# Kernel optimization log

Hardware: AMD Instinct MI355X
Metric: run time of the kernel (lower is better)

Reference implementation:

```python
import jax, jax.numpy as jnp
import numpy as np

# Dimensions
NT, NS = 1000, 2048   # timesteps, basins
NF, NG = 6, 32        # forcing channels, static attributes
NH, NR, HS = 16, 8, 256  # buckets, routing taps, hidden size
NK, NGD = 3, 9        # len(kDict)=3 (km,ki,ke), len(gDict)=9


def setup_inputs() -> dict:
    key = jax.random.key(0)
    ks = jax.random.split(key, 16)
    # Physically plausible forcings: Prcp/Evp nonnegative, T1<=T2 (min/max temp)
    Prcp = jax.random.uniform(ks[0], (NT, NS)) * 10.0
    Evp = jax.random.uniform(ks[1], (NT, NS)) * 5.0
    Tm = jax.random.normal(ks[2], (NT, NS)) * 10.0
    T1 = Tm - jax.random.uniform(ks[3], (NT, NS)) * 5.0
    T2 = Tm + jax.random.uniform(ks[4], (NT, NS)) * 5.0
    Rad = jax.random.uniform(ks[5], (NT, NS))
    Hum = jax.random.uniform(ks[6], (NT, NS))
    x = jnp.stack([Prcp, Evp, T1, T2, Rad, Hum], axis=-1)  # [nt, ns, 6]
    xc = jax.random.normal(ks[7], (NS, NG))

    def lin(k, fan_in, fan_out, s=0.05):
        k1, k2 = jax.random.split(k)
        return (jax.random.normal(k1, (fan_in, fan_out)) * s,
                jax.random.normal(k2, (fan_out,)) * s)

    W_fc, b_fc = lin(ks[8], NG, HS)
    W_r, b_r = lin(ks[9], HS, NH * (NR + 1))
    W_g, b_g = lin(ks[10], HS, NH * NGD)
    W_kin, b_kin = lin(ks[11], 4, HS)
    W_kout, b_kout = lin(ks[12], HS, NH * NK)
    return dict(x=x, xc=xc, W_fc=W_fc, b_fc=b_fc, W_r=W_r, b_r=b_r,
                W_g=W_g, b_g=b_g, W_kin=W_kin, b_kin=b_kin,
                W_kout=W_kout, b_kout=b_kout)


def _hardsigmoid(v):
    return jnp.clip(v / 6.0 + 0.5, 0.0, 1.0)


def _forward(x, xc, W_fc, b_fc, W_r, b_r, W_g, b_g, W_kin, b_kin, W_kout, b_kout):
    nt, ns, _ = x.shape
    Prcp, Evp, T1, T2 = x[..., 0], x[..., 1], x[..., 2], x[..., 3]
    f = x[..., 2:]                        # [nt, ns, 4] (T1,T2,Rad,Hum)

    # ---- getParam (eval mode: DropMask is identity) ----
    state = xc @ W_fc + b_fc              # [ns, hs]
    pK = jnp.tanh(f @ W_kin + b_kin + state) @ W_kout + b_kout  # [nt, ns, nh*3]
    hG = jnp.tanh(state)
    pG = hG @ W_g + b_g                   # [ns, nh*9]
    pR = hG @ W_r + b_r                   # [ns, nh*(nr+1)]

    # sepParam(K): km=exp, ki=relu, ke=exp  -> time-varying [nt, ns, nh]
    km = jnp.exp(pK[..., 0 * NH:1 * NH])
    ki = jax.nn.relu(pK[..., 1 * NH:2 * NH])
    ke = jnp.exp(pK[..., 2 * NH:3 * NH])

    # sepParam(G): static [ns, nh]
    g = lambda i: pG[..., i * NH:(i + 1) * NH]
    kp = jax.nn.sigmoid(g(0))
    ks_ = jax.nn.sigmoid(g(1))
    kd = jax.nn.sigmoid(g(2))
    gd = jax.nn.sigmoid(g(3))
    gl = (jax.nn.sigmoid(g(4)) * 10.0) ** 3
    qb = jax.nn.relu(g(5)) / 10.0
    ga = jax.nn.softmax(g(6), axis=-1)    # area weights over buckets
    gi = _hardsigmoid(g(7)) / 2.0
    ge = jax.nn.relu(g(8))

    # onePeakWeight: unimodal routing weights [ns, nh, nr]
    r = pR.reshape(ns, NH, NR + 1)
    s = jax.nn.softmax(r, axis=-1)
    c = jnp.cumsum(s, axis=-1)
    w = jnp.minimum(c, 1.0 - c + s)[..., :NR]
    wr = w / jnp.sum(w, axis=-1, keepdims=True)

    # divideP: snow/liquid split from min/max temperature crossing 0 C
    fl = jnp.clip(T2 / (T2 - T1 + 1e-5), 0.0, 1.0)  # liquid fraction
    Pl = (Prcp * fl)[..., None]           # [nt, ns, 1]
    Ps = (Prcp * (1.0 - fl))[..., None]
    Ev = Evp[..., None]

    # ---- bucket.step recurrence over time (the custom-scan hot loop) ----
    def step(carry, inp):
        Sf, Ss, Sg = carry                # each [ns, nh]
        Ps_t, Pl_t, Ev_t, km_t, ki_t, ke_t = inp
        # snow bucket: accumulate, melt capped by degree-day factor km
        Sf = Sf + Ps_t
        qf = jnp.minimum(Sf, km_t)
        Sf = Sf - qf
        # partition inflow: impervious/direct fraction gi
        inflow = qf + Pl_t
        qd = inflow * gi
        Ss = Ss + inflow * (1.0 - gi)
        # evapotranspiration
        E = jnp.minimum(jnp.maximum(Ss, 0.0), Ev_t * ke_t * ge)
        Ss = Ss - E
        # interflow capped by ki
        qi = jnp.minimum(ki_t, jnp.maximum(Ss, 0.0))
        Ss = Ss - qi
        # quick flow above capacity gl, slow drainage below
        qp = kp * jnp.maximum(Ss - gl, 0.0)
        qsa = ks_ * jnp.clip(Ss, 0.0, gl)
        Ss = Ss - qp - qsa
        # deep/groundwater bucket: fraction gd percolates, linear reservoir kd + baseflow qb
        Sg = Sg + qsa * gd
        qg = kd * Sg + qb
        Sg = Sg * (1.0 - kd)
        q = qp + qsa * (1.0 - gd) + qg + qd + qi
        return (Sf, Ss, Sg), q

    init = (jnp.zeros((ns, NH), x.dtype),
            jnp.zeros((ns, NH), x.dtype),
            jnp.zeros((ns, NH), x.dtype))
    _, Qp = jax.lax.scan(step, init, (Ps, Pl, Ev, km, ki, ke))  # [nt, ns, nh]

    # routing: valid temporal convolution with per-bucket unit hydrograph wr
    Tout = nt - NR + 1
    Q = jnp.zeros((Tout, ns, NH), Qp.dtype)
    for rr in range(NR):  # NR is a small fixed constant
        Q = Q + Qp[NR - 1 - rr: nt - rr] * wr[..., rr]
    yOut = jnp.sum(Q * ga, axis=-1)       # [Tout, ns]
    return yOut


def reference(x, xc, W_fc, b_fc, W_r, b_r, W_g, b_g, W_kin, b_kin, W_kout, b_kout):
    return _forward(x, xc, W_fc, b_fc, W_r, b_r, W_g, b_g, W_kin, b_kin, W_kout, b_kout)
```

## Files before the change

kernel.cpp:

```cpp
#include <hip/hip_runtime.h>
#include <hip/hip_bf16.h>

#define NT   1000
#define NS   2048
#define NH   16
#define NR   8
#define HS   256
#define TOUT 993

typedef __attribute__((ext_vector_type(8))) short short8;
typedef __attribute__((ext_vector_type(4))) float f32x4;

__device__ __forceinline__ ushort f2bf(float f) {
    union { float f; unsigned int u; } v; v.f = f;
    unsigned int u = v.u;
    return (ushort)((u + 0x7fffu + ((u >> 16) & 1u)) >> 16);
}
__device__ __forceinline__ float bf2f(ushort u) {
    union { unsigned int i; float f; } v; v.i = ((unsigned int)u) << 16; return v.f;
}
__device__ __forceinline__ unsigned int packbf2(float lo, float hi) {
    union { __hip_bfloat162 b; unsigned int u; } v;
    v.b = __float22bfloat162_rn(make_float2(lo, hi));
    return v.u;
}
__device__ __forceinline__ float sigf(float x) { return 1.f / (1.f + __expf(-x)); }
__device__ __forceinline__ float fast_tanh(float z) {
    float e = exp2f(z * 2.885390082f);
    return 1.f - 2.f * __builtin_amdgcn_rcpf(e + 1.f);
}
template<int CTRL>
__device__ __forceinline__ float dpp_add(float v) {
    int s = __builtin_amdgcn_update_dpp(0, __builtin_bit_cast(int, v), CTRL, 0xf, 0xf, true);
    return v + __builtin_bit_cast(float, s);
}
__device__ __forceinline__ void gll16(const void* g, void* l) {
    __builtin_amdgcn_global_load_lds((const __attribute__((address_space(1))) unsigned int*)g,
                                     (__attribute__((address_space(3))) unsigned int*)l, 16, 0, 0);
}
__device__ __forceinline__ void gll4(const void* g, void* l) {
    __builtin_amdgcn_global_load_lds((const __attribute__((address_space(1))) unsigned int*)g,
                                     (__attribute__((address_space(3))) unsigned int*)l, 4, 0, 0);
}

__global__ __launch_bounds__(256) void kA(
    const float* __restrict__ xc, const float* __restrict__ W_fc, const float* __restrict__ b_fc,
    const float* __restrict__ W_r, const float* __restrict__ b_r,
    const float* __restrict__ W_g, const float* __restrict__ b_g,
    const float* __restrict__ W_kin, const float* __restrict__ b_kin,
    const float* __restrict__ W_kout,
    float* __restrict__ stateK, float* __restrict__ params,
    ushort* __restrict__ Wt_g, ushort* __restrict__ whlo_g)
{
    __shared__ float xcs[32];
    __shared__ float hG[256];
    __shared__ float pGR[288];
    const int s = blockIdx.x, tid = threadIdx.x;

    if (tid < 32) xcs[tid] = xc[s * 32 + tid];
    __syncthreads();

    float acc = b_fc[tid];
#pragma unroll 8
    for (int k = 0; k < 32; ++k) acc = fmaf(xcs[k], W_fc[k * 256 + tid], acc);
    stateK[s * 256 + tid] = acc + b_kin[tid];
    hG[tid] = tanhf(acc);
    __syncthreads();

    for (int j = tid; j < 288; j += 256) {
        const float* W = (j < 144) ? W_g : W_r;
        const float* b = (j < 144) ? b_g : b_r;
        int col = (j < 144) ? j : (j - 144);
        float a = b[col];
#pragma unroll 4
        for (int k = 0; k < 256; ++k) a = fmaf(hG[k], W[k * 144 + col], a);
        pGR[j] = a;
    }
    __syncthreads();

    if (tid < 16) {
        const int h = tid;
        float g0 = pGR[h],       g1 = pGR[16 + h],  g2 = pGR[32 + h];
        float g3 = pGR[48 + h],  g4 = pGR[64 + h],  g5 = pGR[80 + h];
        float g6 = pGR[96 + h],  g7 = pGR[112 + h], g8 = pGR[128 + h];
        float kp = sigf(g0), ksg = sigf(g1), kd = sigf(g2), gd = sigf(g3);
        float t4 = sigf(g4) * 10.f; float gl = t4 * t4 * t4;
        float qb = fmaxf(g5, 0.f) * 0.1f;
        float gi = fminf(fmaxf(g7 * (1.f / 6.f) + 0.5f, 0.f), 1.f) * 0.5f;
        float ge = fmaxf(g8, 0.f);
        float m = g6;
        for (int o = 1; o < 16; o <<= 1) m = fmaxf(m, __shfl_xor(m, o));
        float e = __expf(g6 - m), esum = e;
        for (int o = 1; o < 16; o <<= 1) esum += __shfl_xor(esum, o);
        float ga = e / esum;
        float r[9], rm = -1e30f;
#pragma unroll
        for (int i = 0; i < 9; ++i) { r[i] = pGR[144 + h * 9 + i]; rm = fmaxf(rm, r[i]); }
        float er[9], es = 0.f;
#pragma unroll
        for (int i = 0; i < 9; ++i) { er[i] = __expf(r[i] - rm); es += er[i]; }
        float inv_es = 1.f / es, c = 0.f, wsum = 0.f, w[8];
#pragma unroll
        for (int i = 0; i < 8; ++i) {
            float si = er[i] * inv_es; c += si;
            float wi = fminf(c, 1.f - c + si);
            w[i] = wi; wsum += wi;
        }
        const int base = s * 16 + h;
        params[0 * 32768 + base] = kp;       params[1 * 32768 + base] = ksg;
        params[2 * 32768 + base] = kd;       params[3 * 32768 + base] = gd;
        params[4 * 32768 + base] = gl;       params[5 * 32768 + base] = qb;
        params[6 * 32768 + base] = gi;       params[7 * 32768 + base] = 1.f - gi;
        params[8 * 32768 + base] = 1.f - kd; params[9 * 32768 + base] = 1.f - gd;
        params[10 * 32768 + base] = ge;
        float sc = ga / wsum;
#pragma unroll
        for (int i = 0; i < 8; ++i) params[(11 + i) * 32768 + base] = w[i] * sc;
    }

    if (s == 0) {
        for (int i = tid; i < 48 * 256; i += 256) {
            int col = i % 48, slot = i / 48;
            int kk = slot >> 5, q = (slot >> 3) & 3, j = slot & 7;
            int h = kk * 32 + ((j < 4) ? (q * 4 + j) : (16 + q * 4 + (j - 4)));
            Wt_g[col * 264 + slot] = f2bf(W_kout[h * 48 + col]);
        }
        {
            const int h = tid;
#pragma unroll
            for (int f = 0; f < 4; ++f) {
                float w = W_kin[f * 256 + h];
                ushort hi = f2bf(w);
                float lo = w - bf2f(hi);
                whlo_g[h * 8 + f] = hi;
                whlo_g[h * 8 + 4 + f] = f2bf(lo);
            }
        }
    }
}

__global__ __launch_bounds__(256, 3) void kB(
    const float* __restrict__ x,
    const float* __restrict__ stateK, const float* __restrict__ b_kout,
    const ushort* __restrict__ Wt_g, const ushort* __restrict__ whlo_g,
    const float* __restrict__ params,
    unsigned int* __restrict__ kmki, ushort* __restrict__ kevA,
    float2* __restrict__ pspl)
{
    __shared__ ushort Wt[48 * 264];
    __shared__ float  stS[16 * 260];
    __shared__ ushort whloS[2048];
    __shared__ float  geS[256];
    __shared__ float  evS[4][5][16];
    const int tid = threadIdx.x;
    const int st = blockIdx.x & 127;
    const int tg = blockIdx.x >> 7;
    const int s0 = st << 4;

    for (int i = tid; i < 3168; i += 256)
        ((uint2*)Wt)[i] = ((const uint2*)Wt_g)[i];
#pragma unroll
    for (int i = tid; i < 1024; i += 256) {
        int row = i >> 6, c = (i & 63) << 2;
        *(float4*)(stS + row * 260 + c) = *(const float4*)(stateK + (s0 + row) * 256 + c);
    }
    *(float4*)(whloS + tid * 8) = ((const float4*)whlo_g)[tid];
    geS[tid] = params[10 * 32768 + s0 * 16 + tid];
    __syncthreads();

    const int wv = tid >> 6, lane = tid & 63;
    const int mi = lane & 15, quad = lane >> 4;
    const int site = s0 + mi;
    const int t0 = tg * 20 + wv * 5;

    float xf[5][4];
#pragma unroll
    for (int ti = 0; ti < 5; ++ti) {
        const int t = t0 + ti;
        const int xb = (t * 2048 + site) * 6;
        float2 u23 = *(const float2*)(x + xb + 2);
        float2 u45 = *(const float2*)(x + xb + 4);
        xf[ti][0] = u23.x; xf[ti][1] = u23.y; xf[ti][2] = u45.x; xf[ti][3] = u45.y;
        if (lane < 16) {
            float2 u01 = *(const float2*)(x + xb);
            float fl = fminf(fmaxf(u23.y * __builtin_amdgcn_rcpf(u23.y - u23.x + 1e-5f), 0.f), 1.f);
            const int sg = st * 4 + (mi >> 2), sl = mi & 3;
            pspl[(sg * 1000 + t) * 4 + sl] = make_float2(u01.x * (1.f - fl), u01.x * fl);
            evS[wv][ti][mi] = u01.y;
        }
    }

    unsigned int bfr[5][4];
#pragma unroll
    for (int ti = 0; ti < 5; ++ti) {
        const float x0 = xf[ti][0], x1 = xf[ti][1], x2 = xf[ti][2], x3 = xf[ti][3];
        unsigned int h01 = packbf2(x0, x1), h23 = packbf2(x2, x3);
        float l0 = x0 - bf2f((ushort)(h01 & 0xffffu));
        float l1 = x1 - bf2f((ushort)(h01 >> 16));
        float l2 = x2 - bf2f((ushort)(h23 & 0xffffu));
        float l3 = x3 - bf2f((ushort)(h23 >> 16));
        unsigned int l01 = packbf2(l0, l1), l23 = packbf2(l2, l3);
        bfr[ti][0] = (quad == 0) ? h01 : (quad == 1 ? l01 : 0u);
        bfr[ti][1] = (quad == 0) ? h23 : (quad == 1 ? l23 : 0u);
        bfr[ti][2] = (quad == 0) ? h01 : 0u;
        bfr[ti][3] = (quad == 0) ? h23 : 0u;
    }

    const float*  stp = stS + mi * 260;
    const ushort* Wt0 = Wt + mi * 264 + quad * 8;
    const int q4 = quad * 4;

    f32x4 acc[5][3];
#pragma unroll
    for (int ti = 0; ti < 5; ++ti)
#pragma unroll
        for (int j = 0; j < 3; ++j) acc[ti][j] = (f32x4){0.f, 0.f, 0.f, 0.f};

#pragma unroll 1
    for (int kk = 0; kk < 8; ++kk) {
        const int ko = kk * 32;
        union { short8 s; unsigned int u[4]; } W0, W1, A0, A1;
        W0.s = *(const short8*)(whloS + (ko + mi) * 8);
        W1.s = *(const short8*)(whloS + (ko + 16 + mi) * 8);
        A0.u[0] = (quad <= 1) ? W0.u[0] : 0u;
        A0.u[1] = (quad <= 1) ? W0.u[1] : 0u;
        A0.u[2] = (quad == 0) ? W0.u[2] : 0u;
        A0.u[3] = (quad == 0) ? W0.u[3] : 0u;
        A1.u[0] = (quad <= 1) ? W1.u[0] : 0u;
        A1.u[1] = (quad <= 1) ? W1.u[1] : 0u;
        A1.u[2] = (quad == 0) ? W1.u[2] : 0u;
        A1.u[3] = (quad == 0) ? W1.u[3] : 0u;
        f32x4 c0 = *(const f32x4*)(stp + ko + q4);
        f32x4 c1 = *(const f32x4*)(stp + ko + 16 + q4);
        short8 b0 = *(const short8*)(Wt0 + ko);
        short8 b1 = *(const short8*)(Wt0 + 16 * 264 + ko);
        short8 b2 = *(const short8*)(Wt0 + 32 * 264 + ko);
#pragma unroll
        for (int ti = 0; ti < 5; ++ti) {
            union { short8 s; unsigned int u[4]; } B;
            B.u[0] = bfr[ti][0]; B.u[1] = bfr[ti][1];
            B.u[2] = bfr[ti][2]; B.u[3] = bfr[ti][3];
            f32x4 z0 = __builtin_amdgcn_mfma_f32_16x16x32_bf16(A0.s, B.s, c0, 0, 0, 0);
            f32x4 z1 = __builtin_amdgcn_mfma_f32_16x16x32_bf16(A1.s, B.s, c1, 0, 0, 0);
            union { short8 s; unsigned int u[4]; } a;
            a.u[0] = packbf2(fast_tanh(z0[0]), fast_tanh(z0[1]));
            a.u[1] = packbf2(fast_tanh(z0[2]), fast_tanh(z0[3]));
            a.u[2] = packbf2(fast_tanh(z1[0]), fast_tanh(z1[1]));
            a.u[3] = packbf2(fast_tanh(z1[2]), fast_tanh(z1[3]));
            acc[ti][0] = __builtin_amdgcn_mfma_f32_16x16x32_bf16(a.s, b0, acc[ti][0], 0, 0, 0);
            acc[ti][1] = __builtin_amdgcn_mfma_f32_16x16x32_bf16(a.s, b1, acc[ti][1], 0, 0, 0);
            acc[ti][2] = __builtin_amdgcn_mfma_f32_16x16x32_bf16(a.s, b2, acc[ti][2], 0, 0, 0);
        }
    }

    const float bo0 = b_kout[mi], bo1 = b_kout[16 + mi], bo2 = b_kout[32 + mi];
#pragma unroll
    for (int ti = 0; ti < 5; ++ti) {
        const int t = t0 + ti;
#pragma unroll
        for (int reg = 0; reg < 4; ++reg) {
            const int sl = quad * 4 + reg;
            float km = __expf(acc[ti][0][reg] + bo0);
            float ki = fmaxf(acc[ti][1][reg] + bo1, 0.f);
            float ke = __expf(acc[ti][2][reg] + bo2);
            float kev = ke * evS[wv][ti][sl] * geS[sl * 16 + mi];
            const int idx = ((s0 + sl) * 1000 + t) * 16 + mi;
            kmki[idx] = (unsigned int)f2bf(km) | ((unsigned int)f2bf(ki) << 16);
            kevA[idx] = f2bf(kev);
        }
    }
}

#define KM_STRIDE 4160
#define KE_BASE   16640
#define KE_STRIDE 2080
#define PS_BASE   24960
#define BUF_SZ    27008
__global__ __launch_bounds__(64, 1) void kC(
    const unsigned int* __restrict__ kmki, const ushort* __restrict__ kevA,
    const float2* __restrict__ pspl,
    const float* __restrict__ params, float* __restrict__ yOut)
{
    __shared__ char lds[2 * BUF_SZ];
    const int tid = threadIdx.x;
    const int sg = blockIdx.x;
    const int sl = tid >> 4;
    const int s = sg * 4 + sl;
    const int h = tid & 15;
    const int gid = s * 16 + h;

    const float kp  = params[0 * 32768 + gid];
    const float ks_ = params[1 * 32768 + gid];
    const float kd  = params[2 * 32768 + gid];
    const float gd  = params[3 * 32768 + gid];
    const float gl  = params[4 * 32768 + gid];
    const float qbv = params[5 * 32768 + gid];
    const float gi  = params[6 * 32768 + gid];
    const float gi1 = params[7 * 32768 + gid];
    const float kd1 = params[8 * 32768 + gid];
    const float gd1 = params[9 * 32768 + gid];
    float wrga[8];
#pragma unroll
    for (int i = 0; i < 8; ++i) wrga[i] = params[(11 + i) * 32768 + gid];

    float Sf = 0.f, Ss = 0.f, Sg = 0.f;
    float qcur[8], qp1[8], qp2[8];
#pragma unroll
    for (int i = 0; i < 8; ++i) { qcur[i] = 0.f; qp1[i] = 0.f; qp2[i] = 0.f; }

    const char* kmG = (const char*)kmki;
    const char* keG = (const char*)kevA;
    const char* psG = (const char*)pspl;

#define STAGE(c, TAIL) do {                                                     \
        char* L = lds + ((c) & 1) * BUF_SZ;                                     \
        _Pragma("unroll")                                                       \
        for (int q = 0; q < 4; ++q) {                                           \
            const char* gk = kmG + ((size_t)(sg * 4 + q) * 1000 + (c) * 64) * 64; \
            const char* ge = keG + ((size_t)(sg * 4 + q) * 1000 + (c) * 64) * 32; \
            char* lk = L + q * KM_STRIDE;                                       \
            char* le = L + KE_BASE + q * KE_STRIDE;                             \
            if (!(TAIL)) {                                                      \
                _Pragma("unroll")                                               \
                for (int k = 0; k < 4; ++k) gll16(gk + k * 1024 + tid * 16, lk + k * 1024); \
                _Pragma("unroll")                                               \
                for (int k = 0; k < 2; ++k) gll16(ge + k * 1024 + tid * 16, le + k * 1024); \
            } else {                                                            \
                _Pragma("unroll")                                               \
                for (int k = 0; k < 2; ++k) gll16(gk + k * 1024 + tid * 16, lk + k * 1024); \
                _Pragma("unroll")                                               \
                for (int k = 0; k < 2; ++k) gll4(gk + 2048 + k * 256 + tid * 4, lk + 2048 + k * 256); \
                gll16(ge + tid * 16, le);                                       \
                gll4(ge + 1024 + tid * 4, le + 1024);                           \
            }                                                                   \
        }                                                                       \
        const char* gp = psG + ((size_t)sg * 1000 + (c) * 64) * 32;             \
        char* lp = L + PS_BASE;                                                 \
        if (!(TAIL)) { gll16(gp + tid * 16, lp); gll16(gp + 1024 + tid * 16, lp + 1024); } \
        else         { gll16(gp + tid * 16, lp); gll4(gp + 1024 + tid * 4, lp + 1024); }   \
    } while (0)

#define SCANB(c, sb) do {                                                       \
        const char* L = lds + ((c) & 1) * BUF_SZ;                               \
        const char* lk = L + sl * KM_STRIDE + h * 4 + (sb) * 512;               \
        const char* le = L + KE_BASE + sl * KE_STRIDE + h * 2 + (sb) * 256;     \
        const char* lp = L + PS_BASE + sl * 8 + (sb) * 256;                     \
        unsigned int a[8]; ushort e[8]; float2 p[8];                            \
        _Pragma("unroll")                                                       \
        for (int i = 0; i < 8; ++i) {                                           \
            a[i] = *(const unsigned int*)(lk + i * 64);                         \
            e[i] = *(const ushort*)(le + i * 32);                               \
            p[i] = *(const float2*)(lp + i * 32);                               \
        }                                                                       \
        _Pragma("unroll")                                                       \
        for (int i = 0; i < 8; ++i) {                                           \
            float km = __builtin_bit_cast(float, a[i] << 16);                   \
            float ki = __builtin_bit_cast(float, a[i] & 0xffff0000u);           \
            float kev = __builtin_bit_cast(float, ((unsigned int)e[i]) << 16);  \
            float ps = p[i].x, pl = p[i].y;                                     \
            Sf += ps;                                                           \
            float qf = fminf(Sf, km); Sf -= qf;                                 \
            float inflow = qf + pl;                                             \
            float qd = inflow * gi;                                             \
            Ss = fmaf(inflow, gi1, Ss);                                         \
            float E = fminf(Ss, kev); Ss -= E;                                  \
            float qi = fminf(ki, Ss); Ss -= qi;                                 \
            float qp = kp * fmaxf(Ss - gl, 0.f);                                \
            float qsa = ks_ * fminf(Ss, gl);                                    \
            Ss -= qp + qsa;                                                     \
            Sg = fmaf(qsa, gd, Sg);                                             \
            float qg = fmaf(kd, Sg, qbv);                                       \
            Sg *= kd1;                                                          \
            qcur[i] = fmaf(qsa, gd1, qp) + qg + qd + qi;                        \
        }                                                                       \
    } while (0)

#define CONV_STORE(m) do {                                                      \
        float z[8];                                                             \
        _Pragma("unroll")                                                       \
        for (int i = 0; i < 8; ++i) {                                           \
            float za = wrga[6] * ((i >= 6) ? qp1[i - 6] : qp2[i + 2]);          \
            za = fmaf(wrga[4], (i >= 4) ? qp1[i - 4] : qp2[i + 4], za);         \
            za = fmaf(wrga[2], (i >= 2) ? qp1[i - 2] : qp2[i + 6], za);         \
            za = fmaf(wrga[0], qp1[i], za);                                     \
            float zb = wrga[7] * ((i >= 7) ? qp1[i - 7] : qp2[i + 1]);          \
            zb = fmaf(wrga[5], (i >= 5) ? qp1[i - 5] : qp2[i + 3], zb);         \
            zb = fmaf(wrga[3], (i >= 3) ? qp1[i - 3] : qp2[i + 5], zb);         \
            zb = fmaf(wrga[1], (i >= 1) ? qp1[i - 1] : qp2[i + 7], zb);         \
            z[i] = za + zb;                                                     \
        }                                                                       \
        _Pragma("unroll")                                                       \
        for (int i = 0; i < 8; ++i) z[i] = dpp_add<0xB1>(z[i]);                 \
        _Pragma("unroll")                                                       \
        for (int i = 0; i < 8; ++i) z[i] = dpp_add<0x4E>(z[i]);                 \
        _Pragma("unroll")                                                       \
        for (int i = 0; i < 8; ++i) z[i] = dpp_add<0x141>(z[i]);                \
        _Pragma("unroll")                                                       \
        for (int i = 0; i < 8; ++i) z[i] = dpp_add<0x140>(z[i]);                \
        if (h == 0) {                                                           \
            _Pragma("unroll")                                                   \
            for (int i = 0; i < 8; ++i) {                                       \
                const int t = (m) * 8 + i;                                      \
                if (t >= 7) yOut[(t - 7) * 2048 + s] = z[i];                    \
            }                                                                   \
        }                                                                       \
    } while (0)

    STAGE(0, false);
    int g = 0;
#pragma unroll 1
    for (int c = 0; c < 16; ++c) {
        if (c < 15) {
            if (c + 1 == 15) STAGE(15, true);
            else             STAGE(c + 1, false);
            asm volatile("s_waitcnt vmcnt(26)" ::: "memory");
        } else {
            asm volatile("s_waitcnt vmcnt(0)" ::: "memory");
        }
        const int NSB = (c == 15) ? 5 : 8;
#pragma unroll 1
        for (int sb = 0; sb < NSB; ++sb, ++g) {
            SCANB(c, sb);
            CONV_STORE(g - 1);
#pragma unroll
            for (int i = 0; i < 8; ++i) { qp2[i] = qp1[i]; qp1[i] = qcur[i]; }
        }
        asm volatile("" ::: "memory");
    }
    CONV_STORE(124);
#undef STAGE
#undef SCANB
#undef CONV_STORE
}

extern "C" void kernel_launch(void* const* d_in, const int* in_sizes, int n_in,
                              void* d_out, int out_size, void* d_ws, size_t ws_size,
                              hipStream_t stream) {
    const float* x      = (const float*)d_in[0];
    const float* xc     = (const float*)d_in[1];
    const float* W_fc   = (const float*)d_in[2];
    const float* b_fc   = (const float*)d_in[3];
    const float* W_r    = (const float*)d_in[4];
    const float* b_r    = (const float*)d_in[5];
    const float* W_g    = (const float*)d_in[6];
    const float* b_g    = (const float*)d_in[7];
    const float* W_kin  = (const float*)d_in[8];
    const float* b_kin  = (const float*)d_in[9];
    const float* W_kout = (const float*)d_in[10];
    const float* b_kout = (const float*)d_in[11];
    float* yOut = (float*)d_out;

    char* ws = (char*)d_ws;
    float*  stateK = (float*)(ws + 0);
    float*  params = (float*)(ws + (2 << 20));
    ushort* Wt_g   = (ushort*)(ws + (6 << 20));
    ushort* whlo_g = (ushort*)(ws + (6 << 20) + (64 << 10));
    char*   p      = ws + (6 << 20) + (128 << 10);
    float2* pspl   = (float2*)p;
    unsigned int* kmki = (unsigned int*)(p + 16384000);
    ushort* kevA   = (ushort*)(p + 16384000 + 131072000);

    hipLaunchKernelGGL(kA, dim3(2048), dim3(256), 0, stream,
                       xc, W_fc, b_fc, W_r, b_r, W_g, b_g, W_kin, b_kin, W_kout,
                       stateK, params, Wt_g, whlo_g);
    hipLaunchKernelGGL(kB, dim3(128 * 50), dim3(256), 0, stream,
                       x, stateK, b_kout, Wt_g, whlo_g, params, kmki, kevA, pspl);
    hipLaunchKernelGGL(kC, dim3(512), dim3(64), 0, stream,
                       kmki, kevA, pspl, params, yOut);
}
```

Baseline: 519.3 us.

## Split routing convolution from scan kernel into separate parallel kernel

The scan kernel no longer performs the routing convolution and bucket reduction. Instead it stores raw per-bucket flows in place over the consumed kmki buffer. A new kernel kD then computes the convolution and reduction across many more blocks by splitting time into chunks. The aim is to shorten the serial latency-bound scan loop. The cost is a large extra global write and read of the flows, plus an additional launch.

```diff
diff --git a/kernel.cpp b/kernel.cpp
--- a/kernel.cpp
+++ b/kernel.cpp
@@ -277,9 +277,10 @@
 #define PS_BASE   24960
 #define BUF_SZ    27008
 __global__ __launch_bounds__(64, 1) void kC(
-    const unsigned int* __restrict__ kmki, const ushort* __restrict__ kevA,
+    const unsigned int* kmki,
+    const ushort* __restrict__ kevA,
     const float2* __restrict__ pspl,
-    const float* __restrict__ params, float* __restrict__ yOut)
+    const float* __restrict__ params, float* qOut)
 {
     __shared__ char lds[2 * BUF_SZ];
     const int tid = threadIdx.x;
@@ -299,14 +300,11 @@
     const float gi1 = params[7 * 32768 + gid];
     const float kd1 = params[8 * 32768 + gid];
     const float gd1 = params[9 * 32768 + gid];
-    float wrga[8];
-#pragma unroll
-    for (int i = 0; i < 8; ++i) wrga[i] = params[(11 + i) * 32768 + gid];
 
     float Sf = 0.f, Ss = 0.f, Sg = 0.f;
-    float qcur[8], qp1[8], qp2[8];
-#pragma unroll
-    for (int i = 0; i < 8; ++i) { qcur[i] = 0.f; qp1[i] = 0.f; qp2[i] = 0.f; }
+    float qcur[8];
+#pragma unroll
+    for (int i = 0; i < 8; ++i) qcur[i] = 0.f;
 
     const char* kmG = (const char*)kmki;
     const char* keG = (const char*)kevA;
@@ -375,39 +373,14 @@
         }                                                                       \
     } while (0)
 
-#define CONV_STORE(m) do {                                                      \
-        float z[8];                                                             \
+#define STOREQ(c, sb) do {                                                      \
+        const int tb = (c) * 64 + (sb) * 8;                                     \
         _Pragma("unroll")                                                       \
-        for (int i = 0; i < 8; ++i) {                                           \
-            float za = wrga[6] * ((i >= 6) ? qp1[i - 6] : qp2[i + 2]);          \
-            za = fmaf(wrga[4], (i >= 4) ? qp1[i - 4] : qp2[i + 4], za);         \
-            za = fmaf(wrga[2], (i >= 2) ? qp1[i - 2] : qp2[i + 6], za);         \
-            za = fmaf(wrga[0], qp1[i], za);                                     \
-            float zb = wrga[7] * ((i >= 7) ? qp1[i - 7] : qp2[i + 1]);          \
-            zb = fmaf(wrga[5], (i >= 5) ? qp1[i - 5] : qp2[i + 3], zb);         \
-            zb = fmaf(wrga[3], (i >= 3) ? qp1[i - 3] : qp2[i + 5], zb);         \
-            zb = fmaf(wrga[1], (i >= 1) ? qp1[i - 1] : qp2[i + 7], zb);         \
-            z[i] = za + zb;                                                     \
-        }                                                                       \
-        _Pragma("unroll")                                                       \
-        for (int i = 0; i < 8; ++i) z[i] = dpp_add<0xB1>(z[i]);                 \
-        _Pragma("unroll")                                                       \
-        for (int i = 0; i < 8; ++i) z[i] = dpp_add<0x4E>(z[i]);                 \
-        _Pragma("unroll")                                                       \
-        for (int i = 0; i < 8; ++i) z[i] = dpp_add<0x141>(z[i]);                \
-        _Pragma("unroll")                                                       \
-        for (int i = 0; i < 8; ++i) z[i] = dpp_add<0x140>(z[i]);                \
-        if (h == 0) {                                                           \
-            _Pragma("unroll")                                                   \
-            for (int i = 0; i < 8; ++i) {                                       \
-                const int t = (m) * 8 + i;                                      \
-                if (t >= 7) yOut[(t - 7) * 2048 + s] = z[i];                    \
-            }                                                                   \
-        }                                                                       \
+        for (int i = 0; i < 8; ++i)                                             \
+            qOut[(size_t)s * 16000 + (size_t)(tb + i) * 16 + h] = qcur[i];      \
     } while (0)
 
     STAGE(0, false);
-    int g = 0;
 #pragma unroll 1
     for (int c = 0; c < 16; ++c) {
         if (c < 15) {
@@ -419,18 +392,78 @@
         }
         const int NSB = (c == 15) ? 5 : 8;
 #pragma unroll 1
-        for (int sb = 0; sb < NSB; ++sb, ++g) {
+        for (int sb = 0; sb < NSB; ++sb) {
             SCANB(c, sb);
-            CONV_STORE(g - 1);
-#pragma unroll
-            for (int i = 0; i < 8; ++i) { qp2[i] = qp1[i]; qp1[i] = qcur[i]; }
+            STOREQ(c, sb);
         }
         asm volatile("" ::: "memory");
     }
-    CONV_STORE(124);
 #undef STAGE
 #undef SCANB
-#undef CONV_STORE
+#undef STOREQ
+}
+
+__global__ __launch_bounds__(64) void kD(
+    const float* qOut,
+    const float* __restrict__ params, float* __restrict__ yOut)
+{
+    const int tid = threadIdx.x;
+    const int sg = blockIdx.x >> 3;
+    const int tc = blockIdx.x & 7;
+    const int sl = tid >> 4, h = tid & 15;
+    const int s = sg * 4 + sl;
+    const int gid = s * 16 + h;
+    float wrga[8];
+#pragma unroll
+    for (int i = 0; i < 8; ++i) wrga[i] = params[(11 + i) * 32768 + gid];
+    const size_t sbase = (size_t)s * 16000;
+    const int t0 = tc * 128;
+
+    float qprev[8], qcur[8];
+#pragma unroll
+    for (int i = 0; i < 8; ++i) {
+        int t = t0 - 8 + i; t = (t < 0) ? 0 : t;
+        qprev[i] = qOut[sbase + (size_t)t * 16 + h];
+    }
+#pragma unroll 1
+    for (int b = 0; b < 16; ++b) {
+        const int tb = t0 + b * 8;
+#pragma unroll
+        for (int i = 0; i < 8; ++i) {
+            int t = tb + i; t = (t > 999) ? 999 : t;
+            qcur[i] = qOut[sbase + (size_t)t * 16 + h];
+        }
+        float z[8];
+#pragma unroll
+        for (int i = 0; i < 8; ++i) {
+            float za = wrga[6] * ((i >= 6) ? qcur[i - 6] : qprev[i + 2]);
+            za = fmaf(wrga[4], (i >= 4) ? qcur[i - 4] : qprev[i + 4], za);
+            za = fmaf(wrga[2], (i >= 2) ? qcur[i - 2] : qprev[i + 6], za);
+            za = fmaf(wrga[0], qcur[i], za);
+            float zb = wrga[7] * ((i >= 7) ? qcur[i - 7] : qprev[i + 1]);
+            zb = fmaf(wrga[5], (i >= 5) ? qcur[i - 5] : qprev[i + 3], zb);
+            zb = fmaf(wrga[3], (i >= 3) ? qcur[i - 3] : qprev[i + 5], zb);
+            zb = fmaf(wrga[1], (i >= 1) ? qcur[i - 1] : qprev[i + 7], zb);
+            z[i] = za + zb;
+        }
+#pragma unroll
+        for (int i = 0; i < 8; ++i) z[i] = dpp_add<0xB1>(z[i]);
+#pragma unroll
+        for (int i = 0; i < 8; ++i) z[i] = dpp_add<0x4E>(z[i]);
+#pragma unroll
+        for (int i = 0; i < 8; ++i) z[i] = dpp_add<0x141>(z[i]);
+#pragma unroll
+        for (int i = 0; i < 8; ++i) z[i] = dpp_add<0x140>(z[i]);
+        if (h == 0) {
+#pragma unroll
+            for (int i = 0; i < 8; ++i) {
+                const int t = tb + i;
+                if (t >= 7 && t < 1000) yOut[(t - 7) * 2048 + s] = z[i];
+            }
+        }
+#pragma unroll
+        for (int i = 0; i < 8; ++i) qprev[i] = qcur[i];
+    }
 }
 
 extern "C" void kernel_launch(void* const* d_in, const int* in_sizes, int n_in,
@@ -466,5 +499,7 @@
     hipLaunchKernelGGL(kB, dim3(128 * 50), dim3(256), 0, stream,
                        x, stateK, b_kout, Wt_g, whlo_g, params, kmki, kevA, pspl);
     hipLaunchKernelGGL(kC, dim3(512), dim3(64), 0, stream,
-                       kmki, kevA, pspl, params, yOut);
-}
+                       kmki, kevA, pspl, params, (float*)kmki);
+    hipLaunchKernelGGL(kD, dim3(4096), dim3(64), 0, stream,
+                       (const float*)kmki, params, yOut);
+}
```

After: 517.2 us. About the same (-0.4%).

## Split parameter kernel and compute hG·[W_g|W_r] with split-bf16 MFMA

Applied to the files above, without the earlier changes.

The per-basin parameter kernel is split into three kernels. A weight-prep kernel converts W_g/W_r into hi/lo bf16 MFMA fragments, a state kernel produces hG as hi/lo bf16, and a batched kernel runs the 256x288 projection for 16 basins per block with three MFMAs per k-chunk to approximate fp32 precision. This replaces a scalar fp32 dot-product loop that re-read the whole weight matrix for every basin and used only 16 threads for the epilogue. In exchange it adds two launches, borrows scratch space inside the kmki buffer before kB overwrites it, and is slightly less exact than fp32.

```diff
diff --git a/kernel.cpp b/kernel.cpp
--- a/kernel.cpp
+++ b/kernel.cpp
@@ -43,100 +43,149 @@
                                      (__attribute__((address_space(3))) unsigned int*)l, 4, 0, 0);
 }
 
-__global__ __launch_bounds__(256) void kA(
-    const float* __restrict__ xc, const float* __restrict__ W_fc, const float* __restrict__ b_fc,
-    const float* __restrict__ W_r, const float* __restrict__ b_r,
-    const float* __restrict__ W_g, const float* __restrict__ b_g,
-    const float* __restrict__ W_kin, const float* __restrict__ b_kin,
-    const float* __restrict__ W_kout,
-    float* __restrict__ stateK, float* __restrict__ params,
+
+__global__ __launch_bounds__(256) void kAw(
+    const float* __restrict__ W_g, const float* __restrict__ W_r,
+    const float* __restrict__ W_kin, const float* __restrict__ W_kout,
+    ushort* __restrict__ WAhi, ushort* __restrict__ WAlo,
     ushort* __restrict__ Wt_g, ushort* __restrict__ whlo_g)
 {
+    const int tid = threadIdx.x, b = blockIdx.x;
+    const int idx = b * 256 + tid;
+    const int j = idx & 7, lane = (idx >> 3) & 63, chunk = idx >> 9;
+    const int kc = chunk & 7, ct = chunk >> 3;
+    const int col = ct * 16 + (lane & 15);
+    const int k = kc * 32 + (lane >> 4) * 8 + j;
+    const float* W = (col < 144) ? W_g : W_r;
+    const int c2 = (col < 144) ? col : col - 144;
+    const float w = W[k * 144 + c2];
+    const ushort hi = f2bf(w);
+    WAhi[idx] = hi;
+    WAlo[idx] = f2bf(w - bf2f(hi));
+
+    if (b == 0) {
+        for (int i = tid; i < 48 * 256; i += 256) {
+            int c = i % 48, slot = i / 48;
+            int kk2 = slot >> 5, q = (slot >> 3) & 3, jj = slot & 7;
+            int h = kk2 * 32 + ((jj < 4) ? (q * 4 + jj) : (16 + q * 4 + (jj - 4)));
+            Wt_g[c * 264 + slot] = f2bf(W_kout[h * 48 + c]);
+        }
+        const int h = tid;
+#pragma unroll
+        for (int f = 0; f < 4; ++f) {
+            float w2 = W_kin[f * 256 + h];
+            ushort hi2 = f2bf(w2);
+            whlo_g[h * 8 + f] = hi2;
+            whlo_g[h * 8 + 4 + f] = f2bf(w2 - bf2f(hi2));
+        }
+    }
+}
+
+__global__ __launch_bounds__(256) void kA1(
+    const float* __restrict__ xc, const float* __restrict__ W_fc,
+    const float* __restrict__ b_fc, const float* __restrict__ b_kin,
+    float* __restrict__ stateK, ushort* __restrict__ hGh, ushort* __restrict__ hGl)
+{
     __shared__ float xcs[32];
-    __shared__ float hG[256];
-    __shared__ float pGR[288];
     const int s = blockIdx.x, tid = threadIdx.x;
-
     if (tid < 32) xcs[tid] = xc[s * 32 + tid];
     __syncthreads();
-
     float acc = b_fc[tid];
 #pragma unroll 8
     for (int k = 0; k < 32; ++k) acc = fmaf(xcs[k], W_fc[k * 256 + tid], acc);
     stateK[s * 256 + tid] = acc + b_kin[tid];
-    hG[tid] = tanhf(acc);
+    float hg = tanhf(acc);
+    ushort hi = f2bf(hg);
+    hGh[s * 256 + tid] = hi;
+    hGl[s * 256 + tid] = f2bf(hg - bf2f(hi));
+}
+
+__global__ __launch_bounds__(256) void kA2(
+    const ushort* __restrict__ hGh, const ushort* __restrict__ hGl,
+    const ushort* __restrict__ WAhi, const ushort* __restrict__ WAlo,
+    const float* __restrict__ b_g, const float* __restrict__ b_r,
+    float* __restrict__ params)
+{
+    __shared__ ushort hGhS[16][264];
+    __shared__ ushort hGlS[16][264];
+    __shared__ float  pGRS[16][292];
+    const int tid = threadIdx.x;
+    const int s0 = blockIdx.x * 16;
+
+    for (int i = tid; i < 512; i += 256) {
+        int site = i >> 5, off = (i & 31) * 8;
+        *(uint4*)&hGhS[site][off] = *(const uint4*)&hGh[(s0 + site) * 256 + off];
+        *(uint4*)&hGlS[site][off] = *(const uint4*)&hGl[(s0 + site) * 256 + off];
+    }
     __syncthreads();
 
-    for (int j = tid; j < 288; j += 256) {
-        const float* W = (j < 144) ? W_g : W_r;
-        const float* b = (j < 144) ? b_g : b_r;
-        int col = (j < 144) ? j : (j - 144);
-        float a = b[col];
-#pragma unroll 4
-        for (int k = 0; k < 256; ++k) a = fmaf(hG[k], W[k * 144 + col], a);
-        pGR[j] = a;
+    const int wv = tid >> 6, lane = tid & 63;
+    const int n = lane & 15, q = lane >> 4;
+    for (int ct = wv; ct < 18; ct += 4) {
+        f32x4 acc = (f32x4){0.f, 0.f, 0.f, 0.f};
+#pragma unroll
+        for (int kc = 0; kc < 8; ++kc) {
+            const int fidx = ((ct * 8 + kc) * 64 + lane) * 8;
+            short8 awh = *(const short8*)(WAhi + fidx);
+            short8 awl = *(const short8*)(WAlo + fidx);
+            short8 bhh = *(const short8*)&hGhS[n][kc * 32 + q * 8];
+            short8 bhl = *(const short8*)&hGlS[n][kc * 32 + q * 8];
+            acc = __builtin_amdgcn_mfma_f32_16x16x32_bf16(awh, bhh, acc, 0, 0, 0);
+            acc = __builtin_amdgcn_mfma_f32_16x16x32_bf16(awl, bhh, acc, 0, 0, 0);
+            acc = __builtin_amdgcn_mfma_f32_16x16x32_bf16(awh, bhl, acc, 0, 0, 0);
+        }
+#pragma unroll
+        for (int r = 0; r < 4; ++r) pGRS[n][ct * 16 + q * 4 + r] = acc[r];
     }
     __syncthreads();
 
-    if (tid < 16) {
-        const int h = tid;
-        float g0 = pGR[h],       g1 = pGR[16 + h],  g2 = pGR[32 + h];
-        float g3 = pGR[48 + h],  g4 = pGR[64 + h],  g5 = pGR[80 + h];
-        float g6 = pGR[96 + h],  g7 = pGR[112 + h], g8 = pGR[128 + h];
-        float kp = sigf(g0), ksg = sigf(g1), kd = sigf(g2), gd = sigf(g3);
-        float t4 = sigf(g4) * 10.f; float gl = t4 * t4 * t4;
-        float qb = fmaxf(g5, 0.f) * 0.1f;
-        float gi = fminf(fmaxf(g7 * (1.f / 6.f) + 0.5f, 0.f), 1.f) * 0.5f;
-        float ge = fmaxf(g8, 0.f);
-        float m = g6;
-        for (int o = 1; o < 16; o <<= 1) m = fmaxf(m, __shfl_xor(m, o));
-        float e = __expf(g6 - m), esum = e;
-        for (int o = 1; o < 16; o <<= 1) esum += __shfl_xor(esum, o);
-        float ga = e / esum;
-        float r[9], rm = -1e30f;
-#pragma unroll
-        for (int i = 0; i < 9; ++i) { r[i] = pGR[144 + h * 9 + i]; rm = fmaxf(rm, r[i]); }
-        float er[9], es = 0.f;
-#pragma unroll
-        for (int i = 0; i < 9; ++i) { er[i] = __expf(r[i] - rm); es += er[i]; }
-        float inv_es = 1.f / es, c = 0.f, wsum = 0.f, w[8];
-#pragma unroll
-        for (int i = 0; i < 8; ++i) {
-            float si = er[i] * inv_es; c += si;
-            float wi = fminf(c, 1.f - c + si);
-            w[i] = wi; wsum += wi;
-        }
-        const int base = s * 16 + h;
-        params[0 * 32768 + base] = kp;       params[1 * 32768 + base] = ksg;
-        params[2 * 32768 + base] = kd;       params[3 * 32768 + base] = gd;
-        params[4 * 32768 + base] = gl;       params[5 * 32768 + base] = qb;
-        params[6 * 32768 + base] = gi;       params[7 * 32768 + base] = 1.f - gi;
-        params[8 * 32768 + base] = 1.f - kd; params[9 * 32768 + base] = 1.f - gd;
-        params[10 * 32768 + base] = ge;
-        float sc = ga / wsum;
-#pragma unroll
-        for (int i = 0; i < 8; ++i) params[(11 + i) * 32768 + base] = w[i] * sc;
-    }
-
-    if (s == 0) {
-        for (int i = tid; i < 48 * 256; i += 256) {
-            int col = i % 48, slot = i / 48;
-            int kk = slot >> 5, q = (slot >> 3) & 3, j = slot & 7;
-            int h = kk * 32 + ((j < 4) ? (q * 4 + j) : (16 + q * 4 + (j - 4)));
-            Wt_g[col * 264 + slot] = f2bf(W_kout[h * 48 + col]);
-        }
-        {
-            const int h = tid;
-#pragma unroll
-            for (int f = 0; f < 4; ++f) {
-                float w = W_kin[f * 256 + h];
-                ushort hi = f2bf(w);
-                float lo = w - bf2f(hi);
-                whlo_g[h * 8 + f] = hi;
-                whlo_g[h * 8 + 4 + f] = f2bf(lo);
-            }
-        }
-    }
+    const int sl = tid >> 4, h = tid & 15;
+    const int s = s0 + sl;
+    float g0 = pGRS[sl][0 * 16 + h] + b_g[0 * 16 + h];
+    float g1 = pGRS[sl][1 * 16 + h] + b_g[1 * 16 + h];
+    float g2 = pGRS[sl][2 * 16 + h] + b_g[2 * 16 + h];
+    float g3 = pGRS[sl][3 * 16 + h] + b_g[3 * 16 + h];
+    float g4 = pGRS[sl][4 * 16 + h] + b_g[4 * 16 + h];
+    float g5 = pGRS[sl][5 * 16 + h] + b_g[5 * 16 + h];
+    float g6 = pGRS[sl][6 * 16 + h] + b_g[6 * 16 + h];
+    float g7 = pGRS[sl][7 * 16 + h] + b_g[7 * 16 + h];
+    float g8 = pGRS[sl][8 * 16 + h] + b_g[8 * 16 + h];
+    float kp = sigf(g0), ksg = sigf(g1), kd = sigf(g2), gd = sigf(g3);
+    float t4 = sigf(g4) * 10.f; float gl = t4 * t4 * t4;
+    float qb = fmaxf(g5, 0.f) * 0.1f;
+    float gi = fminf(fmaxf(g7 * (1.f / 6.f) + 0.5f, 0.f), 1.f) * 0.5f;
+    float ge = fmaxf(g8, 0.f);
+    float m = g6;
+    for (int o = 1; o < 16; o <<= 1) m = fmaxf(m, __shfl_xor(m, o));
+    float e = __expf(g6 - m), esum = e;
+    for (int o = 1; o < 16; o <<= 1) esum += __shfl_xor(esum, o);
+    float ga = e / esum;
+    float r9[9], rm = -1e30f;
+#pragma unroll
+    for (int i = 0; i < 9; ++i) {
+        r9[i] = pGRS[sl][144 + h * 9 + i] + b_r[h * 9 + i];
+        rm = fmaxf(rm, r9[i]);
+    }
+    float er[9], es = 0.f;
+#pragma unroll
+    for (int i = 0; i < 9; ++i) { er[i] = __expf(r9[i] - rm); es += er[i]; }
+    float inv_es = 1.f / es, c = 0.f, wsum = 0.f, w[8];
+#pragma unroll
+    for (int i = 0; i < 8; ++i) {
+        float si = er[i] * inv_es; c += si;
+        float wi = fminf(c, 1.f - c + si);
+        w[i] = wi; wsum += wi;
+    }
+    const int base = s * 16 + h;
+    params[0 * 32768 + base] = kp;       params[1 * 32768 + base] = ksg;
+    params[2 * 32768 + base] = kd;       params[3 * 32768 + base] = gd;
+    params[4 * 32768 + base] = gl;       params[5 * 32768 + base] = qb;
+    params[6 * 32768 + base] = gi;       params[7 * 32768 + base] = 1.f - gi;
+    params[8 * 32768 + base] = 1.f - kd; params[9 * 32768 + base] = 1.f - gd;
+    params[10 * 32768 + base] = ge;
+    float sc = ga / wsum;
+#pragma unroll
+    for (int i = 0; i < 8; ++i) params[(11 + i) * 32768 + base] = w[i] * sc;
 }
 
 __global__ __launch_bounds__(256, 3) void kB(
@@ -460,9 +509,17 @@
     unsigned int* kmki = (unsigned int*)(p + 16384000);
     ushort* kevA   = (ushort*)(p + 16384000 + 131072000);
 
-    hipLaunchKernelGGL(kA, dim3(2048), dim3(256), 0, stream,
-                       xc, W_fc, b_fc, W_r, b_r, W_g, b_g, W_kin, b_kin, W_kout,
-                       stateK, params, Wt_g, whlo_g);
+    ushort* hGh  = (ushort*)kmki;
+    ushort* hGl  = hGh + 2048 * 256;
+    ushort* WAhi = hGl + 2048 * 256;
+    ushort* WAlo = WAhi + 73728;
+
+    hipLaunchKernelGGL(kAw, dim3(288), dim3(256), 0, stream,
+                       W_g, W_r, W_kin, W_kout, WAhi, WAlo, Wt_g, whlo_g);
+    hipLaunchKernelGGL(kA1, dim3(2048), dim3(256), 0, stream,
+                       xc, W_fc, b_fc, b_kin, stateK, hGh, hGl);
+    hipLaunchKernelGGL(kA2, dim3(128), dim3(256), 0, stream,
+                       hGh, hGl, WAhi, WAlo, b_g, b_r, params);
     hipLaunchKernelGGL(kB, dim3(128 * 50), dim3(256), 0, stream,
                        x, stateK, b_kout, Wt_g, whlo_g, params, kmki, kevA, pspl);
     hipLaunchKernelGGL(kC, dim3(512), dim3(64), 0, stream,
```

Result: faster. 479.1 us (-7.8%).
